# Kernel optimization log

Measured on AMD Instinct MI355X. Metric: run time of the kernel, lower is better.

The kernel has to match this reference:

```python
import jax, jax.numpy as jnp
import numpy as np

NUM_HEADS = 8
TOPK = 16


def setup_inputs() -> dict:
    key = jax.random.key(0)
    ks = jax.random.split(key, 13)
    B, C, H, W = 2, 512, 64, 64
    Hu, Wu = H // 2, W // 2
    hd = C // NUM_HEADS
    n = lambda k, shape, s=1.0: jax.random.normal(k, shape, dtype=jnp.float32) * s
    return {
        "x": n(ks[0], (B, C, H, W)),
        "upper_feat": n(ks[1], (B, C, Hu, Wu)),
        "gumbel": jax.random.gumbel(ks[2], (B, NUM_HEADS, Hu * Wu), dtype=jnp.float32),
        # 1x1 convs (Conv2d + folded eval-mode BN => weight matrix + bias)
        "q_w": n(ks[3], (C, C), 0.02), "q_b": n(ks[4], (C,), 0.02),
        "kv_w": n(ks[5], (2 * C, C), 0.02), "kv_b": n(ks[6], (2 * C,), 0.02),
        "proj_w": n(ks[7], (C, C), 0.02), "proj_b": n(ks[8], (C,), 0.02),
        # depthwise 7x7 PE conv (groups = C)
        "pe_w": n(ks[9], (C, 1, 7, 7), 0.02), "pe_b": n(ks[10], (C,), 0.02),
        # gate conv1d kernel_size=1: [head_dim, 2*head_dim]
        "gate_w": n(ks[11], (hd, 2 * hd), 0.02), "gate_b": n(ks[12], (hd,), 0.02),
    }


def reference(x, upper_feat, gumbel, q_w, q_b, kv_w, kv_b, proj_w, proj_b,
              pe_w, pe_b, gate_w, gate_b):
    B, C, H, W = x.shape
    hd = C // NUM_HEADS
    Hu, Wu = upper_feat.shape[2], upper_feat.shape[3]
    N, Nu = H * W, Hu * Wu
    scale = hd ** -0.5

    def conv1x1(t, w, b):
        return jnp.einsum('bchw,oc->bohw', t, w) + b[None, :, None, None]

    # coarse attention: q from x, k/v from upper_feat
    q = conv1x1(x, q_w, q_b).reshape(B, NUM_HEADS, hd, N).transpose(0, 1, 3, 2)          # [B,h,N,d]
    kv = conv1x1(upper_feat, kv_w, kv_b).reshape(B, NUM_HEADS, 2 * hd, Nu).transpose(0, 1, 3, 2)
    k, v = kv[..., :hd], kv[..., hd:]                                                    # [B,h,Nu,d]
    sim = jnp.einsum('bhnd,bhmd->bhnm', q, k) * scale                                    # [B,h,N,Nu]
    attn = jax.nn.softmax(sim, axis=-1)
    coarse = jnp.einsum('bhnm,bhmd->bhnd', attn, v)                                      # [B,h,N,d]

    # fine branch: kv from x, top-k token selection via gumbel-softmax scores
    f_kv = conv1x1(x, kv_w, kv_b).reshape(B, NUM_HEADS, 2 * hd, N).transpose(0, 1, 3, 2)
    f_k, f_v = f_kv[..., :hd], f_kv[..., hd:]                                            # [B,h,N,d]

    # heat: channel-mean of x, adaptive-avg-pooled 2x2 to upper resolution (no grad)
    heat = jax.lax.stop_gradient(
        x.mean(axis=1).reshape(B, Hu, 2, Wu, 2).mean(axis=(2, 4)).reshape(B, Nu))
    global_sim = sim.mean(axis=2) * heat[:, None, :]                                     # [B,h,Nu]
    soft_weights = jax.nn.softmax(global_sim + gumbel, axis=-1)
    _, idx = jax.lax.top_k(soft_weights, TOPK)                                           # [B,h,K]

    # map each selected upper-token to its 2x2 block of x-tokens
    h_idx = (idx // Wu) * 2
    w_idx = (idx % Wu) * 2
    idx_full = jnp.concatenate(
        [(h_idx + dh) * W + (w_idx + dw) for dh in range(2) for dw in range(2)], axis=-1)  # [B,h,4K]

    topk_k = jnp.take_along_axis(f_k, idx_full[..., None], axis=2)                       # [B,h,4K,d]
    topk_v = jnp.take_along_axis(f_v, idx_full[..., None], axis=2)
    fine = jax.nn.softmax(jnp.einsum('bhnd,bhmd->bhnm', q, topk_k) * scale, axis=-1)
    refined = jnp.einsum('bhnm,bhmd->bhnd', fine, topk_v)                                # [B,h,N,d]

    # gated fusion (conv1d kernel_size=1 == per-token linear over 2d channels)
    fusion = jnp.concatenate([coarse, refined], axis=-1)                                 # [B,h,N,2d]
    gate = jax.nn.sigmoid(jnp.einsum('bhnc,oc->bhno', fusion, gate_w) + gate_b)
    out = gate * refined + (1.0 - gate) * coarse                                         # [B,h,N,d]

    x_out = out.transpose(0, 1, 3, 2).reshape(B, C, H, W)

    # positional encoding: depthwise 7x7 conv on v, bilinear upsample to (H,W)
    v_rs = v.transpose(0, 1, 3, 2).reshape(B, C, Hu, Wu)
    v_pe = jax.lax.conv_general_dilated(
        v_rs, pe_w, (1, 1), ((3, 3), (3, 3)), feature_group_count=C,
        dimension_numbers=('NCHW', 'OIHW', 'NCHW')) + pe_b[None, :, None, None]
    v_pe = jax.image.resize(v_pe, (B, C, H, W), method='bilinear')

    return conv1x1(x_out + v_pe, proj_w, proj_b)
```

## Files before the change

kernel.cpp:

```cpp
#include <hip/hip_runtime.h>
#include <hip/hip_bf16.h>
#include <cstdint>

typedef __hip_bfloat16 bf16;
typedef unsigned short u16;
typedef __attribute__((ext_vector_type(8))) short bf16x8;
typedef __attribute__((ext_vector_type(4))) float f32x4;

static __device__ __forceinline__ float bs2f(u16 s) {
  unsigned int u = ((unsigned int)s) << 16;
  float f;
  __builtin_memcpy(&f, &u, 4);
  return f;
}
static __device__ __forceinline__ u16 f2bs(float f) {
  bf16 h = __float2bfloat16(f);
  u16 s;
  __builtin_memcpy(&s, &h, 2);
  return s;
}
static __device__ __forceinline__ float ldf(const void* p, size_t i, int f32) {
  return f32 ? ((const float*)p)[i] : bs2f(((const u16*)p)[i]);
}

__global__ __launch_bounds__(256) void detect_dtype(const uint4* __restrict__ xs,
                                                    int* __restrict__ flag) {
  int i = blockIdx.x * 256 + threadIdx.x;
  uint4 v = xs[i];
  bool hit = false;
#pragma unroll
  for (int j = 0; j < 4; ++j) {
    unsigned w = (j == 0) ? v.x : (j == 1) ? v.y : (j == 2) ? v.z : v.w;
    if ((w & 0x7F80u) == 0x7F80u) hit = true;
    if ((w & 0x7F800000u) == 0x7F800000u) hit = true;
  }
  unsigned long long mask = __ballot(hit);
  if (mask != 0ull && (threadIdx.x & 63) == 0) atomicOr(flag, 1);
}

__global__ __launch_bounds__(256) void prep_gate(
    const void* __restrict__ gate_w, const void* __restrict__ gate_b,
    u16* __restrict__ gwb, float* __restrict__ gbf,
    const int* __restrict__ dtf) {
  const int f32 = *dtf;
  int t = threadIdx.x;
  for (int i = t; i < 8192; i += 256)
    gwb[i] = f32 ? f2bs(((const float*)gate_w)[i]) : ((const u16*)gate_w)[i];
  if (t < 64) gbf[t] = ldf(gate_b, t, f32);
}

__global__ __launch_bounds__(256) void transpose_bf16(
    const void* __restrict__ src, u16* __restrict__ dst, int N,
    float* __restrict__ heat, const int* __restrict__ dtf) {
  const int f32 = *dtf;
  const int b = blockIdx.z, n0 = blockIdx.x * 64, c0 = blockIdx.y * 64;
  const int t = threadIdx.x;
  __shared__ __align__(16) u16 tile[64][72];
#pragma unroll
  for (int j = 0; j < 2; ++j) {
    int cc = (t >> 3) + j * 32;
    int nn = (t & 7) * 8;
    u16 tmp[8];
    if (f32) {
      const float* s4 = (const float*)src + ((size_t)(b * 512 + c0 + cc)) * N + n0 + nn;
#pragma unroll
      for (int u = 0; u < 8; ++u) tmp[u] = f2bs(s4[u]);
    } else {
      *reinterpret_cast<uint4*>(tmp) = *reinterpret_cast<const uint4*>(
          (const u16*)src + ((size_t)(b * 512 + c0 + cc)) * N + n0 + nn);
    }
    *reinterpret_cast<uint4*>(&tile[cc][nn]) = *reinterpret_cast<const uint4*>(tmp);
  }
  __syncthreads();
  if (heat != nullptr && t < 32) {
    float s = 0.f;
#pragma unroll 8
    for (int cc = 0; cc < 64; ++cc)
      s += bs2f(tile[cc][2 * t]) + bs2f(tile[cc][2 * t + 1]);
    int y = blockIdx.x;
    atomicAdd(&heat[b * 1024 + (y >> 1) * 32 + t], s);
  }
#pragma unroll
  for (int j = 0; j < 2; ++j) {
    int nn = (t >> 3) + j * 32;
    int cc0 = (t & 7) * 8;
    u16 tmp[8];
#pragma unroll
    for (int u = 0; u < 8; ++u) tmp[u] = tile[cc0 + u][nn];
    *reinterpret_cast<uint4*>(&dst[((size_t)b * N + n0 + nn) * 512 + c0 + cc0]) =
        *reinterpret_cast<const uint4*>(tmp);
  }
}

template<int MODE>
__global__ __launch_bounds__(256) void gemm128(
    const u16* __restrict__ A, const void* __restrict__ W,
    const void* __restrict__ bias, u16* __restrict__ o0,
    void* __restrict__ ob, float* __restrict__ qsum, int M,
    const int* __restrict__ dtf) {
  const int f32 = *dtf;
  const int b = blockIdx.z, m0 = blockIdx.x * 128, oo0 = blockIdx.y * 64;
  const int t = threadIdx.x, w = t >> 6, lane = t & 63;
  const int quad = lane >> 4, c = lane & 15;
  __shared__ __align__(16) u16 As[128][72];
  __shared__ __align__(16) u16 Ws[64][72];
  f32x4 acc[2][4];
#pragma unroll
  for (int nt = 0; nt < 2; ++nt)
#pragma unroll
    for (int ot = 0; ot < 4; ++ot) acc[nt][ot] = (f32x4){0.f, 0.f, 0.f, 0.f};
  const u16* Ab = A + (size_t)b * M * 512;
  const int arow = t >> 1, acol = (t & 1) * 32;
  const int wrow = t >> 2, wcol = (t & 3) * 16;

  for (int k0 = 0; k0 < 512; k0 += 64) {
    __syncthreads();
    {
      const u16* ga = Ab + (size_t)(m0 + arow) * 512 + k0 + acol;
      uint4* ad = reinterpret_cast<uint4*>(&As[arow][acol]);
      const uint4* gs = reinterpret_cast<const uint4*>(ga);
      ad[0] = gs[0]; ad[1] = gs[1]; ad[2] = gs[2]; ad[3] = gs[3];
      if (f32) {
        const float* gw = (const float*)W + (size_t)(oo0 + wrow) * 512 + k0 + wcol;
#pragma unroll
        for (int e = 0; e < 16; ++e) Ws[wrow][wcol + e] = f2bs(gw[e]);
      } else {
        const u16* gw = (const u16*)W + (size_t)(oo0 + wrow) * 512 + k0 + wcol;
        *reinterpret_cast<uint4*>(&Ws[wrow][wcol])     = *reinterpret_cast<const uint4*>(gw);
        *reinterpret_cast<uint4*>(&Ws[wrow][wcol + 8]) = *reinterpret_cast<const uint4*>(gw + 8);
      }
    }
    __syncthreads();
#pragma unroll
    for (int ks = 0; ks < 2; ++ks) {
      bf16x8 av[2];
      av[0] = *reinterpret_cast<const bf16x8*>(&As[w * 32 + c][ks * 32 + quad * 8]);
      av[1] = *reinterpret_cast<const bf16x8*>(&As[w * 32 + 16 + c][ks * 32 + quad * 8]);
#pragma unroll
      for (int ot = 0; ot < 4; ++ot) {
        bf16x8 wv = *reinterpret_cast<const bf16x8*>(&Ws[ot * 16 + c][ks * 32 + quad * 8]);
#pragma unroll
        for (int nt = 0; nt < 2; ++nt) {
          if (MODE == 3)
            acc[nt][ot] = __builtin_amdgcn_mfma_f32_16x16x32_bf16(wv, av[nt], acc[nt][ot], 0, 0, 0);
          else
            acc[nt][ot] = __builtin_amdgcn_mfma_f32_16x16x32_bf16(av[nt], wv, acc[nt][ot], 0, 0, 0);
        }
      }
    }
  }

  if (MODE == 0) {
    const int h = oo0 >> 6, bh = b * 8 + h;
#pragma unroll
    for (int ot = 0; ot < 4; ++ot) {
      int o = oo0 + ot * 16 + c;
      int d = o & 63;
      float bv = ldf(bias, o, f32);
      float qs = 0.f;
#pragma unroll
      for (int nt = 0; nt < 2; ++nt)
#pragma unroll
        for (int r = 0; r < 4; ++r) {
          int m = m0 + w * 32 + nt * 16 + quad * 4 + r;
          u16 val = f2bs(acc[nt][ot][r] + bv);
          o0[((size_t)bh * M + m) * 64 + d] = val;
          qs += bs2f(val);
        }
      qs += __shfl_xor(qs, 16, 64);
      qs += __shfl_xor(qs, 32, 64);
      if (quad == 0) atomicAdd(&qsum[bh * 64 + d], qs);
    }
  } else {
#pragma unroll
    for (int ot = 0; ot < 4; ++ot)
#pragma unroll
      for (int r = 0; r < 4; ++r) {
        int o = oo0 + ot * 16 + quad * 4 + r;
        float bv = ldf(bias, o, f32);
#pragma unroll
        for (int nt = 0; nt < 2; ++nt) {
          int m = m0 + w * 32 + nt * 16 + c;
          float val = acc[nt][ot][r] + bv;
          size_t oi_ = ((size_t)(b * 512 + o)) * M + m;
          if (f32) ((float*)ob)[oi_] = val;
          else     ((u16*)ob)[oi_] = f2bs(val);
        }
      }
  }
}

__global__ __launch_bounds__(256) void gemm_kv(
    const u16* __restrict__ A, const void* __restrict__ W,
    const void* __restrict__ bias, u16* __restrict__ kb, u16* __restrict__ vTb,
    int M, const int* __restrict__ dtf) {
  const int f32 = *dtf;
  const int b = blockIdx.z, m0 = blockIdx.x * 64, oo0 = blockIdx.y * 64;
  const int t = threadIdx.x, w = t >> 6, lane = t & 63;
  const int quad = lane >> 4, c = lane & 15;
  __shared__ __align__(16) u16 As[64][72];
  __shared__ __align__(16) u16 Ws[64][72];
  f32x4 acc[4];
#pragma unroll
  for (int ot = 0; ot < 4; ++ot) acc[ot] = (f32x4){0.f, 0.f, 0.f, 0.f};
  const u16* Ab = A + (size_t)b * M * 512;
  const int srow = t >> 2, scol = (t & 3) * 16;

  for (int k0 = 0; k0 < 512; k0 += 64) {
    __syncthreads();
    {
      const u16* ga = Ab + (size_t)(m0 + srow) * 512 + k0 + scol;
      *reinterpret_cast<uint4*>(&As[srow][scol])     = *reinterpret_cast<const uint4*>(ga);
      *reinterpret_cast<uint4*>(&As[srow][scol + 8]) = *reinterpret_cast<const uint4*>(ga + 8);
      if (f32) {
        const float* gw = (const float*)W + (size_t)(oo0 + srow) * 512 + k0 + scol;
#pragma unroll
        for (int e = 0; e < 16; ++e) Ws[srow][scol + e] = f2bs(gw[e]);
      } else {
        const u16* gw = (const u16*)W + (size_t)(oo0 + srow) * 512 + k0 + scol;
        *reinterpret_cast<uint4*>(&Ws[srow][scol])     = *reinterpret_cast<const uint4*>(gw);
        *reinterpret_cast<uint4*>(&Ws[srow][scol + 8]) = *reinterpret_cast<const uint4*>(gw + 8);
      }
    }
    __syncthreads();
#pragma unroll
    for (int ks = 0; ks < 2; ++ks) {
      bf16x8 av = *reinterpret_cast<const bf16x8*>(&As[w * 16 + c][ks * 32 + quad * 8]);
#pragma unroll
      for (int ot = 0; ot < 4; ++ot) {
        bf16x8 wv = *reinterpret_cast<const bf16x8*>(&Ws[ot * 16 + c][ks * 32 + quad * 8]);
        acc[ot] = __builtin_amdgcn_mfma_f32_16x16x32_bf16(av, wv, acc[ot], 0, 0, 0);
      }
    }
  }

#pragma unroll
  for (int ot = 0; ot < 4; ++ot) {
    int o = oo0 + ot * 16 + c;
    float bv = ldf(bias, o, f32);
    int hh = o >> 7, jj = o & 127;
#pragma unroll
    for (int r = 0; r < 4; ++r) {
      int m = m0 + w * 16 + quad * 4 + r;
      u16 val = f2bs(acc[ot][r] + bv);
      if (jj < 64) kb[((size_t)(b * 8 + hh) * M + m) * 64 + jj] = val;
      else         vTb[((size_t)(b * 8 + hh) * 64 + (jj & 63)) * M + m] = val;
    }
  }
}

__global__ __launch_bounds__(256) void topk_kernel(
    const float* __restrict__ qsum, const u16* __restrict__ k,
    const float* __restrict__ heat, const void* __restrict__ gumbel,
    int* __restrict__ posb, const int* __restrict__ dtf) {
  const int f32 = *dtf;
  int bh = blockIdx.x, b = bh >> 3, t = threadIdx.x;
  __shared__ float qs[64];
  __shared__ float s[1024];
  __shared__ float rv[256];
  __shared__ int   ri[256];
  if (t < 64) qs[t] = qsum[bh * 64 + t];
  __syncthreads();
  for (int j = 0; j < 4; ++j) {
    int m = t + j * 256;
    const u16* kr = k + ((size_t)bh * 1024 + m) * 64;
    float dot = 0.f;
    for (int d = 0; d < 64; ++d) dot += qs[d] * bs2f(kr[d]);
    s[m] = dot * (0.125f / 4096.0f) * (heat[b * 1024 + m] * (1.0f / 2048.0f)) +
           ldf(gumbel, (size_t)bh * 1024 + m, f32);
  }
  __syncthreads();
  for (int it = 0; it < 16; ++it) {
    float bv = -1e30f; int bi = 0x7fffffff;
    for (int j = 0; j < 4; ++j) {
      int m = t + j * 256; float vv = s[m];
      if (vv > bv || (vv == bv && m < bi)) { bv = vv; bi = m; }
    }
    rv[t] = bv; ri[t] = bi; __syncthreads();
    for (int off = 128; off; off >>= 1) {
      if (t < off) {
        if (rv[t + off] > rv[t] || (rv[t + off] == rv[t] && ri[t + off] < ri[t])) {
          rv[t] = rv[t + off]; ri[t] = ri[t + off];
        }
      }
      __syncthreads();
    }
    if (t == 0) {
      int mi = ri[0]; s[mi] = -1e30f;
      int hy = (mi >> 5) * 2, wx = (mi & 31) * 2;
      posb[bh * 64 + it]      = hy * 64 + wx;
      posb[bh * 64 + 16 + it] = hy * 64 + wx + 1;
      posb[bh * 64 + 32 + it] = (hy + 1) * 64 + wx;
      posb[bh * 64 + 48 + it] = (hy + 1) * 64 + wx + 1;
    }
    __syncthreads();
  }
}

__global__ __launch_bounds__(256) void gather_kv_mfma(
    const u16* __restrict__ xT, const void* __restrict__ kv_w,
    const void* __restrict__ kv_b, const int* __restrict__ posb,
    u16* __restrict__ tkb, u16* __restrict__ tvTb,
    const int* __restrict__ dtf) {
  const int f32 = *dtf;
  const int bh = blockIdx.x, b = bh >> 3, h = bh & 7;
  const int half = blockIdx.y;
  const int t = threadIdx.x, w = t >> 6, lane = t & 63;
  const int quad = lane >> 4, c = lane & 15;
  __shared__ int pos[64];
  __shared__ __align__(16) u16 As[64][72];
  __shared__ __align__(16) u16 Ws[64][72];
  if (t < 64) pos[t] = posb[bh * 64 + t];
  __syncthreads();
  const int obase = h * 128 + half * 64;
  const int srow = t >> 2, scol = (t & 3) * 16;
  const int arow = pos[srow];
  f32x4 acc[4];
#pragma unroll
  for (int ot = 0; ot < 4; ++ot) acc[ot] = (f32x4){0.f, 0.f, 0.f, 0.f};

  for (int k0 = 0; k0 < 512; k0 += 64) {
    __syncthreads();
    {
      const u16* ga = xT + ((size_t)b * 4096 + arow) * 512 + k0 + scol;
      *reinterpret_cast<uint4*>(&As[srow][scol])     = *reinterpret_cast<const uint4*>(ga);
      *reinterpret_cast<uint4*>(&As[srow][scol + 8]) = *reinterpret_cast<const uint4*>(ga + 8);
      if (f32) {
        const float* gw = (const float*)kv_w + (size_t)(obase + srow) * 512 + k0 + scol;
#pragma unroll
        for (int e = 0; e < 16; ++e) Ws[srow][scol + e] = f2bs(gw[e]);
      } else {
        const u16* gw = (const u16*)kv_w + (size_t)(obase + srow) * 512 + k0 + scol;
        *reinterpret_cast<uint4*>(&Ws[srow][scol])     = *reinterpret_cast<const uint4*>(gw);
        *reinterpret_cast<uint4*>(&Ws[srow][scol + 8]) = *reinterpret_cast<const uint4*>(gw + 8);
      }
    }
    __syncthreads();
#pragma unroll
    for (int ks = 0; ks < 2; ++ks) {
      bf16x8 av = *reinterpret_cast<const bf16x8*>(&As[w * 16 + c][ks * 32 + quad * 8]);
#pragma unroll
      for (int ot = 0; ot < 4; ++ot) {
        bf16x8 wv = *reinterpret_cast<const bf16x8*>(&Ws[ot * 16 + c][ks * 32 + quad * 8]);
        acc[ot] = __builtin_amdgcn_mfma_f32_16x16x32_bf16(av, wv, acc[ot], 0, 0, 0);
      }
    }
  }

#pragma unroll
  for (int ot = 0; ot < 4; ++ot) {
    int d = ot * 16 + c;
    float bv = ldf(kv_b, obase + d, f32);
#pragma unroll
    for (int r = 0; r < 4; ++r) {
      int m = w * 16 + quad * 4 + r;
      u16 val = f2bs(acc[ot][r] + bv);
      if (half) tvTb[((size_t)bh * 64 + d) * 64 + m] = val;
      else      tkb[((size_t)bh * 64 + m) * 64 + d] = val;
    }
  }
}

__global__ __launch_bounds__(256) void dwconv_kernel(
    const u16* __restrict__ vT, const void* __restrict__ pe_w,
    const void* __restrict__ pe_b, u16* __restrict__ vpe,
    const int* __restrict__ dtf) {
  const int f32 = *dtf;
  int bc = blockIdx.x;
  int b = bc >> 9, c = bc & 511;
  int h = c >> 6, d = c & 63;
  int t = threadIdx.x;
  __shared__ float img[1024];
  __shared__ float wts[49];
  const u16* base = vT + ((size_t)(b * 8 + h) * 64 + d) * 1024;
  if (t < 128) {
    uint4 v4 = reinterpret_cast<const uint4*>(base)[t];
    u16 tmp[8];
    *reinterpret_cast<uint4*>(tmp) = v4;
#pragma unroll
    for (int e = 0; e < 8; ++e) img[t * 8 + e] = bs2f(tmp[e]);
  }
  if (t < 49) wts[t] = ldf(pe_w, c * 49 + t, f32);
  float bias = ldf(pe_b, c, f32);
  __syncthreads();
  for (int i = t; i < 1024; i += 256) {
    int y = i >> 5, xx = i & 31;
    float a = 0.f;
#pragma unroll
    for (int ky = 0; ky < 7; ++ky) {
      int yy = y + ky - 3;
      if ((unsigned)yy >= 32u) continue;
#pragma unroll
      for (int kx = 0; kx < 7; ++kx) {
        int xc = xx + kx - 3;
        if ((unsigned)xc >= 32u) continue;
        a += img[yy * 32 + xc] * wts[ky * 7 + kx];
      }
    }
    vpe[(size_t)bc * 1024 + i] = f2bs(a + bias);
  }
}

__global__ __launch_bounds__(256, 4) void attn_fused(
    const u16* __restrict__ q, const u16* __restrict__ k,
    const u16* __restrict__ vT, const u16* __restrict__ tkb,
    const u16* __restrict__ tvTb, const u16* __restrict__ gwb,
    const float* __restrict__ gbf, const u16* __restrict__ vpe,
    u16* __restrict__ xsT) {
  const int bh = blockIdx.y, b = bh >> 3, h = bh & 7;
  const int bx = blockIdx.x;
  const int n0 = bx * 64;
  const int t = threadIdx.x, w = t >> 6, lane = t & 63;
  const int quad = lane >> 4, c = lane & 15;

  __shared__ __align__(16) u16 lds[13824];
  u16* Ks = lds;
  u16* Vt = lds + 4608;
  u16* Ps = lds + 9216;

  bf16x8 bq[2];
  {
    const u16* qr = q + ((size_t)bh * 4096 + n0 + w * 16 + c) * 64;
    bq[0] = *reinterpret_cast<const bf16x8*>(qr + quad * 8);
    bq[1] = *reinterpret_cast<const bf16x8*>(qr + 32 + quad * 8);
  }
  f32x4 po[4];
#pragma unroll
  for (int dt = 0; dt < 4; ++dt) po[dt] = (f32x4){0.f, 0.f, 0.f, 0.f};
  float sume = 0.f;

  const u16* kbase = k + (size_t)bh * 65536;
  const u16* vbase = vT + (size_t)bh * 65536;
  const int srow = t >> 2, scol = (t & 3) * 16;

  uint4 kr0, kr1, vr0, vr1;
  {
    const u16* gk = kbase + (size_t)srow * 64 + scol;
    kr0 = *reinterpret_cast<const uint4*>(gk);
    kr1 = *reinterpret_cast<const uint4*>(gk + 8);
    const u16* gv = vbase + (size_t)srow * 1024 + scol;
    vr0 = *reinterpret_cast<const uint4*>(gv);
    vr1 = *reinterpret_cast<const uint4*>(gv + 8);
  }

  for (int ch = 0; ch < 16; ++ch) {
    __syncthreads();
    *reinterpret_cast<uint4*>(&Ks[srow * 72 + scol])     = kr0;
    *reinterpret_cast<uint4*>(&Ks[srow * 72 + scol + 8]) = kr1;
    *reinterpret_cast<uint4*>(&Vt[srow * 72 + scol])     = vr0;
    *reinterpret_cast<uint4*>(&Vt[srow * 72 + scol + 8]) = vr1;
    __syncthreads();
    if (ch + 1 < 16) {
      const int m1 = (ch + 1) * 64;
      const u16* gk = kbase + (size_t)(m1 + srow) * 64 + scol;
      kr0 = *reinterpret_cast<const uint4*>(gk);
      kr1 = *reinterpret_cast<const uint4*>(gk + 8);
      const u16* gv = vbase + (size_t)srow * 1024 + m1 + scol;
      vr0 = *reinterpret_cast<const uint4*>(gv);
      vr1 = *reinterpret_cast<const uint4*>(gv + 8);
    }

    f32x4 st[4];
#pragma unroll
    for (int mt = 0; mt < 4; ++mt) {
      const u16* krow = &Ks[(mt * 16 + c) * 72];
      bf16x8 ak0 = *reinterpret_cast<const bf16x8*>(krow + quad * 8);
      bf16x8 ak1 = *reinterpret_cast<const bf16x8*>(krow + 32 + quad * 8);
      f32x4 acc = (f32x4){0.f, 0.f, 0.f, 0.f};
      acc = __builtin_amdgcn_mfma_f32_16x16x32_bf16(ak0, bq[0], acc, 0, 0, 0);
      acc = __builtin_amdgcn_mfma_f32_16x16x32_bf16(ak1, bq[1], acc, 0, 0, 0);
      st[mt] = acc;
    }
    float cs = 0.f;
    u16* psw = &Ps[(w * 16 + c) * 72];
#pragma unroll
    for (int mt = 0; mt < 4; ++mt) {
      float e0 = __expf(st[mt][0] * 0.125f);
      float e1 = __expf(st[mt][1] * 0.125f);
      float e2 = __expf(st[mt][2] * 0.125f);
      float e3 = __expf(st[mt][3] * 0.125f);
      cs += (e0 + e1) + (e2 + e3);
      ushort4 pw;
      pw.x = f2bs(e0); pw.y = f2bs(e1); pw.z = f2bs(e2); pw.w = f2bs(e3);
      *reinterpret_cast<ushort4*>(psw + mt * 16 + quad * 4) = pw;
    }
    cs += __shfl_xor(cs, 16, 64);
    cs += __shfl_xor(cs, 32, 64);
    sume += cs;
#pragma unroll
    for (int s = 0; s < 2; ++s) {
      bf16x8 bp = *reinterpret_cast<const bf16x8*>(psw + s * 32 + quad * 8);
#pragma unroll
      for (int dt = 0; dt < 4; ++dt) {
        bf16x8 av = *reinterpret_cast<const bf16x8*>(&Vt[(dt * 16 + c) * 72 + s * 32 + quad * 8]);
        po[dt] = __builtin_amdgcn_mfma_f32_16x16x32_bf16(av, bp, po[dt], 0, 0, 0);
      }
    }
  }

  __syncthreads();
  u16* fus = lds;
  u16* vl  = lds + 8704;
  float* gbl = (float*)(lds + 13312);

  const int ym = bx >> 1;
  int r0_, r1_; float wy0, wy1;
  if ((bx & 1) == 0) { r0_ = ym > 0 ? ym - 1 : 0; r1_ = ym; wy0 = 0.25f; wy1 = 0.75f; }
  else               { r0_ = ym; r1_ = ym < 31 ? ym + 1 : 31; wy0 = 0.75f; wy1 = 0.25f; }

  for (int idx = t; idx < 512; idx += 256) {
    int seg = idx & 3, ch2 = (idx >> 2) & 63, rr = idx >> 8;
    int vrow = rr ? r1_ : r0_;
    const uint4 v4 = *reinterpret_cast<const uint4*>(
        vpe + ((size_t)(b * 512 + h * 64 + ch2)) * 1024 + vrow * 32 + seg * 8);
    u16* dst = &vl[(rr * 64 + ch2) * 36 + seg * 8];
    uint2 lo, hi;
    lo.x = v4.x; lo.y = v4.y; hi.x = v4.z; hi.y = v4.w;
    *reinterpret_cast<uint2*>(dst)     = lo;
    *reinterpret_cast<uint2*>(dst + 4) = hi;
  }
  if (t < 64) gbl[t] = gbf[t];
  __syncthreads();

  u16* fusw = &fus[(w * 16 + c) * 136];
  f32x4 st2[4];
#pragma unroll
  for (int mt = 0; mt < 4; ++mt) {
    f32x4 acc = (f32x4){0.f, 0.f, 0.f, 0.f};
#pragma unroll
    for (int s = 0; s < 2; ++s) {
      bf16x8 ak = *reinterpret_cast<const bf16x8*>(
          &tkb[((size_t)bh * 64 + mt * 16 + c) * 64 + s * 32 + quad * 8]);
      acc = __builtin_amdgcn_mfma_f32_16x16x32_bf16(ak, bq[s], acc, 0, 0, 0);
    }
    st2[mt] = acc;
  }
  float sume2 = 0.f;
#pragma unroll
  for (int mt = 0; mt < 4; ++mt) {
    float e0 = __expf(st2[mt][0] * 0.125f);
    float e1 = __expf(st2[mt][1] * 0.125f);
    float e2 = __expf(st2[mt][2] * 0.125f);
    float e3 = __expf(st2[mt][3] * 0.125f);
    sume2 += (e0 + e1) + (e2 + e3);
    ushort4 pw;
    pw.x = f2bs(e0); pw.y = f2bs(e1); pw.z = f2bs(e2); pw.w = f2bs(e3);
    *reinterpret_cast<ushort4*>(fusw + mt * 16 + quad * 4) = pw;
  }
  sume2 += __shfl_xor(sume2, 16, 64);
  sume2 += __shfl_xor(sume2, 32, 64);
  float inv2 = 1.0f / sume2;

  f32x4 po2[4];
#pragma unroll
  for (int dt = 0; dt < 4; ++dt) po2[dt] = (f32x4){0.f, 0.f, 0.f, 0.f};
#pragma unroll
  for (int s = 0; s < 2; ++s) {
    bf16x8 bp = *reinterpret_cast<const bf16x8*>(fusw + s * 32 + quad * 8);
#pragma unroll
    for (int dt = 0; dt < 4; ++dt) {
      bf16x8 av = *reinterpret_cast<const bf16x8*>(
          &tvTb[((size_t)bh * 64 + dt * 16 + c) * 64 + s * 32 + quad * 8]);
      po2[dt] = __builtin_amdgcn_mfma_f32_16x16x32_bf16(av, bp, po2[dt], 0, 0, 0);
    }
  }

  float invc = 1.0f / sume;
#pragma unroll
  for (int dt = 0; dt < 4; ++dt) {
    ushort4 cw, rw;
    cw.x = f2bs(po[dt][0] * invc); cw.y = f2bs(po[dt][1] * invc);
    cw.z = f2bs(po[dt][2] * invc); cw.w = f2bs(po[dt][3] * invc);
    rw.x = f2bs(po2[dt][0] * inv2); rw.y = f2bs(po2[dt][1] * inv2);
    rw.z = f2bs(po2[dt][2] * inv2); rw.w = f2bs(po2[dt][3] * inv2);
    *reinterpret_cast<ushort4*>(fusw + dt * 16 + quad * 4)      = cw;
    *reinterpret_cast<ushort4*>(fusw + 64 + dt * 16 + quad * 4) = rw;
  }

  f32x4 ga[4];
#pragma unroll
  for (int ot = 0; ot < 4; ++ot) ga[ot] = (f32x4){0.f, 0.f, 0.f, 0.f};
#pragma unroll
  for (int s = 0; s < 4; ++s) {
    bf16x8 bf = *reinterpret_cast<const bf16x8*>(fusw + s * 32 + quad * 8);
#pragma unroll
    for (int ot = 0; ot < 4; ++ot) {
      bf16x8 ag = *reinterpret_cast<const bf16x8*>(
          gwb + (ot * 16 + c) * 128 + s * 32 + quad * 8);
      ga[ot] = __builtin_amdgcn_mfma_f32_16x16x32_bf16(ag, bf, ga[ot], 0, 0, 0);
    }
  }

  const int x = w * 16 + c;
  int jx = x >> 1, x0, x1; float wx0, wx1;
  if ((x & 1) == 0) { x0 = (jx > 0) ? jx - 1 : 0; x1 = jx; wx0 = 0.25f; wx1 = 0.75f; }
  else              { x0 = jx; x1 = (jx < 31) ? jx + 1 : 31; wx0 = 0.75f; wx1 = 0.25f; }
#pragma unroll
  for (int dt = 0; dt < 4; ++dt) {
    ushort4 ow;
    u16 tmp[4];
#pragma unroll
    for (int r = 0; r < 4; ++r) {
      int row = dt * 16 + quad * 4 + r;
      float ref = po2[dt][r] * inv2;
      float coar = bs2f(fusw[row]);
      float g = 1.0f / (1.0f + __expf(-(ga[dt][r] + gbl[row])));
      float vv = wy0 * (wx0 * bs2f(vl[row * 36 + x0]) +
                        wx1 * bs2f(vl[row * 36 + x1])) +
                 wy1 * (wx0 * bs2f(vl[(64 + row) * 36 + x0]) +
                        wx1 * bs2f(vl[(64 + row) * 36 + x1]));
      tmp[r] = f2bs(g * ref + (1.0f - g) * coar + vv);
    }
    ow.x = tmp[0]; ow.y = tmp[1]; ow.z = tmp[2]; ow.w = tmp[3];
    *reinterpret_cast<ushort4*>(fusw + dt * 16 + quad * 4) = ow;
  }

  {
    int nl = lane >> 2, cs2 = (lane & 3) * 16;
    const u16* srcrow = &fus[(w * 16 + nl) * 136 + cs2];
    u16* dst = xsT + ((size_t)b * 4096 + n0 + w * 16 + nl) * 512 + h * 64 + cs2;
    *reinterpret_cast<uint4*>(dst)     = *reinterpret_cast<const uint4*>(srcrow);
    *reinterpret_cast<uint4*>(dst + 8) = *reinterpret_cast<const uint4*>(srcrow + 8);
  }
}

extern "C" void kernel_launch(void* const* d_in, const int* in_sizes, int n_in,
                              void* d_out, int out_size, void* d_ws, size_t ws_size,
                              hipStream_t stream) {
  const void* x    = d_in[0];
  const void* up   = d_in[1];
  const void* gum  = d_in[2];
  const void* q_w  = d_in[3];
  const void* q_b  = d_in[4];
  const void* kv_w = d_in[5];
  const void* kv_b = d_in[6];
  const void* p_w  = d_in[7];
  const void* p_b  = d_in[8];
  const void* pe_w = d_in[9];
  const void* pe_b = d_in[10];
  const void* g_w  = d_in[11];
  const void* g_b  = d_in[12];

  float* ws    = (float*)d_ws;
  int*   dtf   = (int*)ws;
  float* qsum  = ws + 16;
  float* heat  = qsum + 1024;
  int*   posb  = (int*)(heat + 2048);
  float* gbf   = (float*)(posb + 1024);
  u16*   gwb   = (u16*)(gbf + 64);
  u16*   tkb   = gwb + 8192;
  u16*   tvTb  = tkb + 65536;
  u16*   qb    = tvTb + 65536;
  u16*   kb    = qb + 4194304;
  u16*   vTb   = kb + 1048576;
  u16*   xT    = vTb + 1048576;
  u16*   upT   = xT + 4194304;
  u16*   xsT   = upT + 1048576;
  u16*   vpe   = xsT + 4194304;

  dim3 blk(256);
  hipMemsetAsync(ws, 0, (16 + 1024 + 2048) * 4, stream);
  detect_dtype<<<dim3(64), blk, 0, stream>>>((const uint4*)x, dtf);
  prep_gate<<<dim3(1), blk, 0, stream>>>(g_w, g_b, gwb, gbf, dtf);
  transpose_bf16<<<dim3(64, 8, 2), blk, 0, stream>>>(x, xT, 4096, heat, dtf);
  transpose_bf16<<<dim3(16, 8, 2), blk, 0, stream>>>(up, upT, 1024, nullptr, dtf);
  gemm128<0><<<dim3(32, 8, 2), blk, 0, stream>>>(xT, q_w, q_b, qb, nullptr, qsum, 4096, dtf);
  gemm_kv<<<dim3(16, 16, 2), blk, 0, stream>>>(upT, kv_w, kv_b, kb, vTb, 1024, dtf);
  topk_kernel<<<dim3(16), blk, 0, stream>>>(qsum, kb, heat, gum, posb, dtf);
  gather_kv_mfma<<<dim3(16, 2), blk, 0, stream>>>(xT, kv_w, kv_b, posb, tkb, tvTb, dtf);
  dwconv_kernel<<<dim3(1024), blk, 0, stream>>>(vTb, pe_w, pe_b, vpe, dtf);
  attn_fused<<<dim3(64, 16), blk, 0, stream>>>(qb, kb, vTb, tkb, tvTb, gwb, gbf, vpe, xsT);
  gemm128<3><<<dim3(32, 8, 2), blk, 0, stream>>>(xsT, p_w, p_b, nullptr, d_out, nullptr, 4096, dtf);
}
```

Baseline: 262.5 us.

## Pre-swizzle V into MFMA fragment layout, double-buffer K tiles, fold softmax scale into Q

```diff
diff --git a/kernel.cpp b/kernel.cpp
--- a/kernel.cpp
+++ b/kernel.cpp
@@ -163,9 +163,9 @@
 #pragma unroll
         for (int r = 0; r < 4; ++r) {
           int m = m0 + w * 32 + nt * 16 + quad * 4 + r;
-          u16 val = f2bs(acc[nt][ot][r] + bv);
-          o0[((size_t)bh * M + m) * 64 + d] = val;
-          qs += bs2f(val);
+          float qv = acc[nt][ot][r] + bv;
+          o0[((size_t)bh * M + m) * 64 + d] = f2bs(qv * 0.125f);
+          qs += qv;
         }
       qs += __shfl_xor(qs, 16, 64);
       qs += __shfl_xor(qs, 32, 64);
@@ -192,7 +192,7 @@
 
 __global__ __launch_bounds__(256) void gemm_kv(
     const u16* __restrict__ A, const void* __restrict__ W,
-    const void* __restrict__ bias, u16* __restrict__ kb, u16* __restrict__ vTb,
+    const void* __restrict__ bias, u16* __restrict__ kb, u16* __restrict__ v2,
     int M, const int* __restrict__ dtf) {
   const int f32 = *dtf;
   const int b = blockIdx.z, m0 = blockIdx.x * 64, oo0 = blockIdx.y * 64;
@@ -243,8 +243,13 @@
     for (int r = 0; r < 4; ++r) {
       int m = m0 + w * 16 + quad * 4 + r;
       u16 val = f2bs(acc[ot][r] + bv);
-      if (jj < 64) kb[((size_t)(b * 8 + hh) * M + m) * 64 + jj] = val;
-      else         vTb[((size_t)(b * 8 + hh) * 64 + (jj & 63)) * M + m] = val;
+      if (jj < 64) {
+        kb[((size_t)(b * 8 + hh) * M + m) * 64 + jj] = val;
+      } else {
+        int d = jj & 63;
+        v2[((((size_t)(b * 8 + hh) * 16 + (m >> 6)) * 2 + ((m >> 5) & 1)) * 4 + (d >> 4)) * 512
+           + (((m >> 3) & 3) * 16 + (d & 15)) * 8 + (m & 7)] = val;
+      }
     }
   }
 }
@@ -362,19 +367,22 @@
 }
 
 __global__ __launch_bounds__(256) void dwconv_kernel(
-    const u16* __restrict__ vT, const void* __restrict__ pe_w,
+    const u16* __restrict__ v2, const void* __restrict__ pe_w,
     const void* __restrict__ pe_b, u16* __restrict__ vpe,
     const int* __restrict__ dtf) {
   const int f32 = *dtf;
   int bc = blockIdx.x;
   int b = bc >> 9, c = bc & 511;
   int h = c >> 6, d = c & 63;
+  int dt = d >> 4, cc = d & 15;
   int t = threadIdx.x;
   __shared__ float img[1024];
   __shared__ float wts[49];
-  const u16* base = vT + ((size_t)(b * 8 + h) * 64 + d) * 1024;
   if (t < 128) {
-    uint4 v4 = reinterpret_cast<const uint4*>(base)[t];
+    int ch = t >> 3, s = (t >> 2) & 1, q2 = t & 3;
+    const u16* src = v2 + ((((size_t)(b * 8 + h) * 16 + ch) * 2 + s) * 4 + dt) * 512
+                        + (q2 * 16 + cc) * 8;
+    uint4 v4 = *reinterpret_cast<const uint4*>(src);
     u16 tmp[8];
     *reinterpret_cast<uint4*>(tmp) = v4;
 #pragma unroll
@@ -403,7 +411,7 @@
 
 __global__ __launch_bounds__(256, 4) void attn_fused(
     const u16* __restrict__ q, const u16* __restrict__ k,
-    const u16* __restrict__ vT, const u16* __restrict__ tkb,
+    const u16* __restrict__ v2, const u16* __restrict__ tkb,
     const u16* __restrict__ tvTb, const u16* __restrict__ gwb,
     const float* __restrict__ gbf, const u16* __restrict__ vpe,
     u16* __restrict__ xsT) {
@@ -415,7 +423,6 @@
 
   __shared__ __align__(16) u16 lds[13824];
   u16* Ks = lds;
-  u16* Vt = lds + 4608;
   u16* Ps = lds + 9216;
 
   bf16x8 bq[2];
@@ -430,40 +437,39 @@
   float sume = 0.f;
 
   const u16* kbase = k + (size_t)bh * 65536;
-  const u16* vbase = vT + (size_t)bh * 65536;
+  const u16* v2base = v2 + (size_t)bh * 65536;
   const int srow = t >> 2, scol = (t & 3) * 16;
 
-  uint4 kr0, kr1, vr0, vr1;
+  uint4 kr0, kr1;
   {
     const u16* gk = kbase + (size_t)srow * 64 + scol;
     kr0 = *reinterpret_cast<const uint4*>(gk);
     kr1 = *reinterpret_cast<const uint4*>(gk + 8);
-    const u16* gv = vbase + (size_t)srow * 1024 + scol;
-    vr0 = *reinterpret_cast<const uint4*>(gv);
-    vr1 = *reinterpret_cast<const uint4*>(gv + 8);
-  }
-
-  for (int ch = 0; ch < 16; ++ch) {
-    __syncthreads();
     *reinterpret_cast<uint4*>(&Ks[srow * 72 + scol])     = kr0;
     *reinterpret_cast<uint4*>(&Ks[srow * 72 + scol + 8]) = kr1;
-    *reinterpret_cast<uint4*>(&Vt[srow * 72 + scol])     = vr0;
-    *reinterpret_cast<uint4*>(&Vt[srow * 72 + scol + 8]) = vr1;
-    __syncthreads();
-    if (ch + 1 < 16) {
-      const int m1 = (ch + 1) * 64;
-      const u16* gk = kbase + (size_t)(m1 + srow) * 64 + scol;
-      kr0 = *reinterpret_cast<const uint4*>(gk);
-      kr1 = *reinterpret_cast<const uint4*>(gk + 8);
-      const u16* gv = vbase + (size_t)srow * 1024 + m1 + scol;
-      vr0 = *reinterpret_cast<const uint4*>(gv);
-      vr1 = *reinterpret_cast<const uint4*>(gv + 8);
+    const u16* gk1 = kbase + (size_t)(64 + srow) * 64 + scol;
+    kr0 = *reinterpret_cast<const uint4*>(gk1);
+    kr1 = *reinterpret_cast<const uint4*>(gk1 + 8);
+  }
+
+  for (int ch = 0; ch < 16; ++ch) {
+    __syncthreads();
+    const int buf = ch & 1;
+
+    bf16x8 av[4][2];
+    {
+      const u16* v2c = v2base + (size_t)ch * 4096;
+#pragma unroll
+      for (int dt = 0; dt < 4; ++dt) {
+        av[dt][0] = *reinterpret_cast<const bf16x8*>(v2c + dt * 512 + lane * 8);
+        av[dt][1] = *reinterpret_cast<const bf16x8*>(v2c + 2048 + dt * 512 + lane * 8);
+      }
     }
 
     f32x4 st[4];
 #pragma unroll
     for (int mt = 0; mt < 4; ++mt) {
-      const u16* krow = &Ks[(mt * 16 + c) * 72];
+      const u16* krow = &Ks[buf * 4608 + (mt * 16 + c) * 72];
       bf16x8 ak0 = *reinterpret_cast<const bf16x8*>(krow + quad * 8);
       bf16x8 ak1 = *reinterpret_cast<const bf16x8*>(krow + 32 + quad * 8);
       f32x4 acc = (f32x4){0.f, 0.f, 0.f, 0.f};
@@ -471,14 +477,25 @@
       acc = __builtin_amdgcn_mfma_f32_16x16x32_bf16(ak1, bq[1], acc, 0, 0, 0);
       st[mt] = acc;
     }
+
+    if (ch + 1 < 16) {
+      *reinterpret_cast<uint4*>(&Ks[(buf ^ 1) * 4608 + srow * 72 + scol])     = kr0;
+      *reinterpret_cast<uint4*>(&Ks[(buf ^ 1) * 4608 + srow * 72 + scol + 8]) = kr1;
+      if (ch + 2 < 16) {
+        const u16* gk = kbase + (size_t)((ch + 2) * 64 + srow) * 64 + scol;
+        kr0 = *reinterpret_cast<const uint4*>(gk);
+        kr1 = *reinterpret_cast<const uint4*>(gk + 8);
+      }
+    }
+
     float cs = 0.f;
     u16* psw = &Ps[(w * 16 + c) * 72];
 #pragma unroll
     for (int mt = 0; mt < 4; ++mt) {
-      float e0 = __expf(st[mt][0] * 0.125f);
-      float e1 = __expf(st[mt][1] * 0.125f);
-      float e2 = __expf(st[mt][2] * 0.125f);
-      float e3 = __expf(st[mt][3] * 0.125f);
+      float e0 = __expf(st[mt][0]);
+      float e1 = __expf(st[mt][1]);
+      float e2 = __expf(st[mt][2]);
+      float e3 = __expf(st[mt][3]);
       cs += (e0 + e1) + (e2 + e3);
       ushort4 pw;
       pw.x = f2bs(e0); pw.y = f2bs(e1); pw.z = f2bs(e2); pw.w = f2bs(e3);
@@ -487,13 +504,13 @@
     cs += __shfl_xor(cs, 16, 64);
     cs += __shfl_xor(cs, 32, 64);
     sume += cs;
+
 #pragma unroll
     for (int s = 0; s < 2; ++s) {
       bf16x8 bp = *reinterpret_cast<const bf16x8*>(psw + s * 32 + quad * 8);
 #pragma unroll
       for (int dt = 0; dt < 4; ++dt) {
-        bf16x8 av = *reinterpret_cast<const bf16x8*>(&Vt[(dt * 16 + c) * 72 + s * 32 + quad * 8]);
-        po[dt] = __builtin_amdgcn_mfma_f32_16x16x32_bf16(av, bp, po[dt], 0, 0, 0);
+        po[dt] = __builtin_amdgcn_mfma_f32_16x16x32_bf16(av[dt][s], bp, po[dt], 0, 0, 0);
       }
     }
   }
@@ -538,10 +555,10 @@
   float sume2 = 0.f;
 #pragma unroll
   for (int mt = 0; mt < 4; ++mt) {
-    float e0 = __expf(st2[mt][0] * 0.125f);
-    float e1 = __expf(st2[mt][1] * 0.125f);
-    float e2 = __expf(st2[mt][2] * 0.125f);
-    float e3 = __expf(st2[mt][3] * 0.125f);
+    float e0 = __expf(st2[mt][0]);
+    float e1 = __expf(st2[mt][1]);
+    float e2 = __expf(st2[mt][2]);
+    float e3 = __expf(st2[mt][3]);
     sume2 += (e0 + e1) + (e2 + e3);
     ushort4 pw;
     pw.x = f2bs(e0); pw.y = f2bs(e1); pw.z = f2bs(e2); pw.w = f2bs(e3);
@@ -652,8 +669,8 @@
   u16*   tvTb  = tkb + 65536;
   u16*   qb    = tvTb + 65536;
   u16*   kb    = qb + 4194304;
-  u16*   vTb   = kb + 1048576;
-  u16*   xT    = vTb + 1048576;
+  u16*   v2b   = kb + 1048576;
+  u16*   xT    = v2b + 1048576;
   u16*   upT   = xT + 4194304;
   u16*   xsT   = upT + 1048576;
   u16*   vpe   = xsT + 4194304;
@@ -665,10 +682,10 @@
   transpose_bf16<<<dim3(64, 8, 2), blk, 0, stream>>>(x, xT, 4096, heat, dtf);
   transpose_bf16<<<dim3(16, 8, 2), blk, 0, stream>>>(up, upT, 1024, nullptr, dtf);
   gemm128<0><<<dim3(32, 8, 2), blk, 0, stream>>>(xT, q_w, q_b, qb, nullptr, qsum, 4096, dtf);
-  gemm_kv<<<dim3(16, 16, 2), blk, 0, stream>>>(upT, kv_w, kv_b, kb, vTb, 1024, dtf);
+  gemm_kv<<<dim3(16, 16, 2), blk, 0, stream>>>(upT, kv_w, kv_b, kb, v2b, 1024, dtf);
   topk_kernel<<<dim3(16), blk, 0, stream>>>(qsum, kb, heat, gum, posb, dtf);
   gather_kv_mfma<<<dim3(16, 2), blk, 0, stream>>>(xT, kv_w, kv_b, posb, tkb, tvTb, dtf);
-  dwconv_kernel<<<dim3(1024), blk, 0, stream>>>(vTb, pe_w, pe_b, vpe, dtf);
-  attn_fused<<<dim3(64, 16), blk, 0, stream>>>(qb, kb, vTb, tkb, tvTb, gwb, gbf, vpe, xsT);
+  dwconv_kernel<<<dim3(1024), blk, 0, stream>>>(v2b, pe_w, pe_b, vpe, dtf);
+  attn_fused<<<dim3(64, 16), blk, 0, stream>>>(qb, kb, v2b, tkb, tvTb, gwb, gbf, vpe, xsT);
   gemm128<3><<<dim3(32, 8, 2), blk, 0, stream>>>(xsT, p_w, p_b, nullptr, d_out, nullptr, 4096, dtf);
 }
```

Measured after the change: 257.2 us. 2.0% less time.
